# Optimization experiments

Hardware: AMD Instinct MI355X
Metric: run time of the kernel (lower is better)

The kernel has to match this reference:

```python
import jax, jax.numpy as jnp
import numpy as np
import math

D_MODEL = 768
B, S = 8, 2048


def setup_inputs() -> dict:
    key = jax.random.key(0)
    k1, k2, k3, k4, k5 = jax.random.split(key, 5)
    return {
        "input": jax.random.normal(k1, (B, S, D_MODEL), dtype=jnp.float32),
        "attention_mask": jax.random.randint(k2, (B,), 0, S + 1, dtype=jnp.int32),
        "Wq": jax.random.normal(k3, (D_MODEL, D_MODEL), dtype=jnp.float32),
        "Wk": jax.random.normal(k4, (D_MODEL, D_MODEL), dtype=jnp.float32),
        "Wv": jax.random.normal(k5, (D_MODEL, D_MODEL), dtype=jnp.float32),
    }


def reference(input, attention_mask, Wq, Wk, Wv):
    d_model = Wq.shape[0]
    # QKV projections (v is computed in the original but never used in the output)
    q = jnp.matmul(input, Wq)  # [B,S,D]
    k = jnp.matmul(input, Wk)  # [B,S,D]
    v = jnp.matmul(input, Wv)  # [B,S,D] (dead in original forward output)
    # Per-sample QK^T, vectorized instead of the original python loop+cat
    attention_score = jnp.einsum("bqd,bkd->bqk", q, k) / math.sqrt(float(d_model) ** 3)
    # Ragged mask: positions (j,k) with j<len_i and k<len_i keep the score, else -1000.
    # Built with vectorized arange comparisons instead of the original triple python loop.
    idx = jnp.arange(attention_score.shape[1])  # [S]
    valid = idx[None, :] < attention_mask[:, None]  # [B,S]
    keep = valid[:, :, None] & valid[:, None, :]  # [B,S,S]
    mask_attention_score = jnp.where(keep, attention_score, jnp.float32(-1000.0))
    attention_score_n = jax.nn.softmax(mask_attention_score, axis=-1)  # computed but unused, as in original
    # Original returns UNMASKED, pre-softmax scores matmul'd with the raw input (not v).
    self_attention = jnp.einsum("bqk,bkd->bqd", attention_score, input)
    return self_attention
```

## Files before the change

kernel.cpp:

```cpp
#include <hip/hip_runtime.h>
#include <hip/hip_bf16.h>
#include <cmath>


typedef __attribute__((ext_vector_type(8))) short short8;
typedef __attribute__((ext_vector_type(4))) float f32x4;

__device__ __forceinline__ unsigned short f2bf(float f) {
    union { float f; unsigned int u; } v; v.f = f;
    unsigned int u = v.u;
    return (unsigned short)((u + 0x7FFFu + ((u >> 16) & 1u)) >> 16);
}

__global__ __launch_bounds__(256)
void transpose_bf16(const float* __restrict__ X, unsigned short* __restrict__ Xt,
                    unsigned short* __restrict__ Xbf, int S, int D)
{
    __shared__ unsigned short tile[32][36];
    const int b = blockIdx.z;
    const int s0 = blockIdx.x * 32;
    const int d0 = blockIdx.y * 32;
    const float* Xb = X + (size_t)b * S * D;
    unsigned short* Xtb = Xt + (size_t)b * S * D;
    unsigned short* Xbb = Xbf + (size_t)b * S * D;
    const int tx = threadIdx.x & 7;
    const int ty = threadIdx.x >> 3;

    float4 v = *reinterpret_cast<const float4*>(&Xb[(size_t)(s0 + ty) * D + d0 + tx * 4]);
    ushort4 pk;
    pk.x = f2bf(v.x); pk.y = f2bf(v.y); pk.z = f2bf(v.z); pk.w = f2bf(v.w);
    *reinterpret_cast<ushort4*>(&Xbb[(size_t)(s0 + ty) * D + d0 + tx * 4]) = pk;
    tile[tx * 4 + 0][ty] = pk.x;
    tile[tx * 4 + 1][ty] = pk.y;
    tile[tx * 4 + 2][ty] = pk.z;
    tile[tx * 4 + 3][ty] = pk.w;
    __syncthreads();
    ushort4 o;
    o.x = tile[ty][tx * 4 + 0];
    o.y = tile[ty][tx * 4 + 1];
    o.z = tile[ty][tx * 4 + 2];
    o.w = tile[ty][tx * 4 + 3];
    *reinterpret_cast<ushort4*>(&Xtb[(size_t)(d0 + ty) * S + s0 + tx * 4]) = o;
}

template <int ROWS>
__device__ __forceinline__ void stage_glds(const unsigned short* src, unsigned short* lds,
                                           int ld, int tid)
{
    #pragma unroll
    for (int it = 0; it < ROWS / 32; ++it) {
        int slot = it * 256 + tid;
        int r = slot >> 3, c = slot & 7;
        const unsigned short* gp = src + (size_t)r * ld + ((c ^ (r & 7)) << 3);
        unsigned short* lp = lds + (size_t)(it * 256 + (tid & 192)) * 8;
        __builtin_amdgcn_global_load_lds(
            (__attribute__((address_space(1))) void*)(void*)gp,
            (__attribute__((address_space(3))) void*)lp, 16, 0, 0);
    }
}

template <int ROWS>
__device__ __forceinline__ void stage_f32(const float* src, unsigned short* lds,
                                          int ld, int tid)
{
    #pragma unroll
    for (int it = 0; it < ROWS / 32; ++it) {
        int slot = it * 256 + tid;
        int r = slot >> 3, c = slot & 7;
        const float* p = src + (size_t)r * ld + ((c ^ (r & 7)) << 3);
        float4 a = *reinterpret_cast<const float4*>(p);
        float4 b = *reinterpret_cast<const float4*>(p + 4);
        uint4 v;
        v.x = (unsigned)f2bf(a.x) | ((unsigned)f2bf(a.y) << 16);
        v.y = (unsigned)f2bf(a.z) | ((unsigned)f2bf(a.w) << 16);
        v.z = (unsigned)f2bf(b.x) | ((unsigned)f2bf(b.y) << 16);
        v.w = (unsigned)f2bf(b.z) | ((unsigned)f2bf(b.w) << 16);
        *reinterpret_cast<uint4*>(&lds[(size_t)slot * 8]) = v;
    }
}

__device__ __forceinline__ void store_c(float* C, size_t i, float v) { C[i] = v; }
__device__ __forceinline__ void store_c(unsigned short* C, size_t i, float v) { C[i] = f2bf(v); }

template <int TM, int TN, bool AF32, bool BF32, typename CT>
__global__ __launch_bounds__(256)
void gemm(const void* __restrict__ Ap, const void* __restrict__ Bp, CT* __restrict__ Cb,
          int Kloop, int lda, int ldb, int ldc, long sA, long sB, long sC, float alpha)
{
    constexpr int FM = TM / 32;
    constexpr int FN = TN / 32;
    const int b = blockIdx.z;
    CT* C = Cb + (long)b * sC;

    __shared__ unsigned short Alds[TM * 64];
    __shared__ unsigned short Blds[TN * 64];

    const int tid  = threadIdx.x;
    const int lane = tid & 63;
    const int wave = tid >> 6;
    const int wr   = (wave >> 1) * (TM / 2);
    const int wc   = (wave & 1) * (TN / 2);
    const int rowBase = blockIdx.x * TM;
    const int colBase = blockIdx.y * TN;
    const int l15  = lane & 15;
    const int quad = lane >> 4;

    f32x4 acc[FM][FN] = {};

    for (int k0 = 0; k0 < Kloop; k0 += 64) {
        if constexpr (AF32)
            stage_f32<TM>((const float*)Ap + (long)b * sA + (size_t)rowBase * lda + k0,
                          Alds, lda, tid);
        else
            stage_glds<TM>((const unsigned short*)Ap + (long)b * sA + (size_t)rowBase * lda + k0,
                           Alds, lda, tid);
        if constexpr (BF32)
            stage_f32<TN>((const float*)Bp + (long)b * sB + (size_t)colBase * ldb + k0,
                          Blds, ldb, tid);
        else
            stage_glds<TN>((const unsigned short*)Bp + (long)b * sB + (size_t)colBase * ldb + k0,
                           Blds, ldb, tid);
        __syncthreads();

        short8 af[FM][2], bfr[FN][2];
        #pragma unroll
        for (int i = 0; i < FM; ++i) {
            int ra = wr + i * 16 + l15;
            af[i][0] = *reinterpret_cast<const short8*>(&Alds[ra * 64 + ((quad ^ (ra & 7)) << 3)]);
            af[i][1] = *reinterpret_cast<const short8*>(&Alds[ra * 64 + (((quad + 4) ^ (ra & 7)) << 3)]);
        }
        #pragma unroll
        for (int i = 0; i < FN; ++i) {
            int rb = wc + i * 16 + l15;
            bfr[i][0] = *reinterpret_cast<const short8*>(&Blds[rb * 64 + ((quad ^ (rb & 7)) << 3)]);
            bfr[i][1] = *reinterpret_cast<const short8*>(&Blds[rb * 64 + (((quad + 4) ^ (rb & 7)) << 3)]);
        }
        #pragma unroll
        for (int ks = 0; ks < 2; ++ks)
            #pragma unroll
            for (int mi = 0; mi < FM; ++mi)
                #pragma unroll
                for (int ni = 0; ni < FN; ++ni)
                    acc[mi][ni] = __builtin_amdgcn_mfma_f32_16x16x32_bf16(
                        af[mi][ks], bfr[ni][ks], acc[mi][ni], 0, 0, 0);
        __syncthreads();
    }

    #pragma unroll
    for (int mi = 0; mi < FM; ++mi) {
        #pragma unroll
        for (int ni = 0; ni < FN; ++ni) {
            int col = colBase + wc + ni * 16 + l15;
            #pragma unroll
            for (int r = 0; r < 4; ++r) {
                int row = rowBase + wr + mi * 16 + quad * 4 + r;
                store_c(C, (size_t)row * ldc + col, alpha * acc[mi][ni][r]);
            }
        }
    }
}

extern "C" void kernel_launch(void* const* d_in, const int* in_sizes, int n_in,
                              void* d_out, int out_size, void* d_ws, size_t ws_size,
                              hipStream_t stream)
{
    const float* X  = (const float*)d_in[0];
    const float* Wq = (const float*)d_in[2];
    const float* Wk = (const float*)d_in[3];
    float* out = (float*)d_out;

    const int Bn = 8, S = 2048, D = 768;
    const float alpha = 1.0f / (768.0f * sqrtf(768.0f));
    const size_t szX  = (size_t)Bn * S * D;
    const size_t szDD = (size_t)Bn * D * D;

    unsigned short* Xt16 = (unsigned short*)d_ws;
    unsigned short* Xbf  = Xt16 + szX;
    unsigned short* P16  = Xbf + szX;
    unsigned short* G16  = P16 + (size_t)D * D;
    unsigned short* Ht16 = G16 + szDD;

    transpose_bf16<<<dim3(S / 32, D / 32, Bn), 256, 0, stream>>>(X, Xt16, Xbf, S, D);

    gemm<64, 64, true, true, unsigned short><<<dim3(12, 12, 1), 256, 0, stream>>>(
        Wq, Wk, P16, D, D, D, D, 0L, 0L, 0L, 1.0f);

    gemm<96, 96, false, false, unsigned short><<<dim3(8, 8, Bn), 256, 0, stream>>>(
        Xt16, Xt16, G16, S, S, S, D, (long)D * S, (long)D * S, (long)D * D, 1.0f);

    gemm<96, 96, false, false, unsigned short><<<dim3(8, 8, Bn), 256, 0, stream>>>(
        G16, P16, Ht16, D, D, D, D, (long)D * D, 0L, (long)D * D, alpha);

    gemm<128, 128, false, false, float><<<dim3(S / 128, 6, Bn), 256, 0, stream>>>(
        Xbf, Ht16, out, D, D, D, D, (long)S * D, (long)D * D, (long)S * D, 1.0f);
}
```

Baseline: 214.8 us.

## Pre-convert weights to bf16 and put batch on grid x for L2 reuse

Adds a separate kernel that converts Wq and Wk to bf16, so the weight-product GEMM can use async global-to-LDS loads instead of loading fp32 and converting inside the GEMM. It also moves the batch index to blockIdx.x so consecutively scheduled workgroups belong to different batches and share the same tile coordinates. The intent is to change how shared operands such as P16 and Ht16 are reused in L2, and to simplify the GEMM template. The cost is one extra launch and more workspace, and the new grid order could hurt locality for the per-batch operands.

```diff
diff --git a/kernel.cpp b/kernel.cpp
--- a/kernel.cpp
+++ b/kernel.cpp
@@ -10,6 +10,28 @@
     union { float f; unsigned int u; } v; v.f = f;
     unsigned int u = v.u;
     return (unsigned short)((u + 0x7FFFu + ((u >> 16) & 1u)) >> 16);
+}
+
+__global__ __launch_bounds__(256)
+void convert_w(const float* __restrict__ Wq, const float* __restrict__ Wk,
+               unsigned short* __restrict__ Wq16, unsigned short* __restrict__ Wk16)
+{
+    int i = (blockIdx.x * 256 + threadIdx.x) * 8;
+    float4 a = *reinterpret_cast<const float4*>(&Wq[i]);
+    float4 b = *reinterpret_cast<const float4*>(&Wq[i + 4]);
+    uint4 v;
+    v.x = (unsigned)f2bf(a.x) | ((unsigned)f2bf(a.y) << 16);
+    v.y = (unsigned)f2bf(a.z) | ((unsigned)f2bf(a.w) << 16);
+    v.z = (unsigned)f2bf(b.x) | ((unsigned)f2bf(b.y) << 16);
+    v.w = (unsigned)f2bf(b.z) | ((unsigned)f2bf(b.w) << 16);
+    *reinterpret_cast<uint4*>(&Wq16[i]) = v;
+    a = *reinterpret_cast<const float4*>(&Wk[i]);
+    b = *reinterpret_cast<const float4*>(&Wk[i + 4]);
+    v.x = (unsigned)f2bf(a.x) | ((unsigned)f2bf(a.y) << 16);
+    v.y = (unsigned)f2bf(a.z) | ((unsigned)f2bf(a.w) << 16);
+    v.z = (unsigned)f2bf(b.x) | ((unsigned)f2bf(b.y) << 16);
+    v.w = (unsigned)f2bf(b.z) | ((unsigned)f2bf(b.w) << 16);
+    *reinterpret_cast<uint4*>(&Wk16[i]) = v;
 }
 
 __global__ __launch_bounds__(256)
@@ -59,37 +81,18 @@
     }
 }
 
-template <int ROWS>
-__device__ __forceinline__ void stage_f32(const float* src, unsigned short* lds,
-                                          int ld, int tid)
-{
-    #pragma unroll
-    for (int it = 0; it < ROWS / 32; ++it) {
-        int slot = it * 256 + tid;
-        int r = slot >> 3, c = slot & 7;
-        const float* p = src + (size_t)r * ld + ((c ^ (r & 7)) << 3);
-        float4 a = *reinterpret_cast<const float4*>(p);
-        float4 b = *reinterpret_cast<const float4*>(p + 4);
-        uint4 v;
-        v.x = (unsigned)f2bf(a.x) | ((unsigned)f2bf(a.y) << 16);
-        v.y = (unsigned)f2bf(a.z) | ((unsigned)f2bf(a.w) << 16);
-        v.z = (unsigned)f2bf(b.x) | ((unsigned)f2bf(b.y) << 16);
-        v.w = (unsigned)f2bf(b.z) | ((unsigned)f2bf(b.w) << 16);
-        *reinterpret_cast<uint4*>(&lds[(size_t)slot * 8]) = v;
-    }
-}
-
 __device__ __forceinline__ void store_c(float* C, size_t i, float v) { C[i] = v; }
 __device__ __forceinline__ void store_c(unsigned short* C, size_t i, float v) { C[i] = f2bf(v); }
 
-template <int TM, int TN, bool AF32, bool BF32, typename CT>
+template <int TM, int TN, typename CT>
 __global__ __launch_bounds__(256)
-void gemm(const void* __restrict__ Ap, const void* __restrict__ Bp, CT* __restrict__ Cb,
+void gemm(const unsigned short* __restrict__ Ap, const unsigned short* __restrict__ Bp,
+          CT* __restrict__ Cb,
           int Kloop, int lda, int ldb, int ldc, long sA, long sB, long sC, float alpha)
 {
     constexpr int FM = TM / 32;
     constexpr int FN = TN / 32;
-    const int b = blockIdx.z;
+    const int b = blockIdx.x;
     CT* C = Cb + (long)b * sC;
 
     __shared__ unsigned short Alds[TM * 64];
@@ -100,26 +103,16 @@
     const int wave = tid >> 6;
     const int wr   = (wave >> 1) * (TM / 2);
     const int wc   = (wave & 1) * (TN / 2);
-    const int rowBase = blockIdx.x * TM;
-    const int colBase = blockIdx.y * TN;
+    const int rowBase = blockIdx.y * TM;
+    const int colBase = blockIdx.z * TN;
     const int l15  = lane & 15;
     const int quad = lane >> 4;
 
     f32x4 acc[FM][FN] = {};
 
     for (int k0 = 0; k0 < Kloop; k0 += 64) {
-        if constexpr (AF32)
-            stage_f32<TM>((const float*)Ap + (long)b * sA + (size_t)rowBase * lda + k0,
-                          Alds, lda, tid);
-        else
-            stage_glds<TM>((const unsigned short*)Ap + (long)b * sA + (size_t)rowBase * lda + k0,
-                           Alds, lda, tid);
-        if constexpr (BF32)
-            stage_f32<TN>((const float*)Bp + (long)b * sB + (size_t)colBase * ldb + k0,
-                          Blds, ldb, tid);
-        else
-            stage_glds<TN>((const unsigned short*)Bp + (long)b * sB + (size_t)colBase * ldb + k0,
-                           Blds, ldb, tid);
+        stage_glds<TM>(Ap + (long)b * sA + (size_t)rowBase * lda + k0, Alds, lda, tid);
+        stage_glds<TN>(Bp + (long)b * sB + (size_t)colBase * ldb + k0, Blds, ldb, tid);
         __syncthreads();
 
         short8 af[FM][2], bfr[FN][2];
@@ -179,18 +172,22 @@
     unsigned short* P16  = Xbf + szX;
     unsigned short* G16  = P16 + (size_t)D * D;
     unsigned short* Ht16 = G16 + szDD;
+    unsigned short* Wq16 = Ht16 + szDD;
+    unsigned short* Wk16 = Wq16 + (size_t)D * D;
+
+    convert_w<<<dim3(D * D / 2048, 1, 1), 256, 0, stream>>>(Wq, Wk, Wq16, Wk16);
 
     transpose_bf16<<<dim3(S / 32, D / 32, Bn), 256, 0, stream>>>(X, Xt16, Xbf, S, D);
 
-    gemm<64, 64, true, true, unsigned short><<<dim3(12, 12, 1), 256, 0, stream>>>(
-        Wq, Wk, P16, D, D, D, D, 0L, 0L, 0L, 1.0f);
+    gemm<64, 64, unsigned short><<<dim3(1, 12, 12), 256, 0, stream>>>(
+        Wq16, Wk16, P16, D, D, D, D, 0L, 0L, 0L, 1.0f);
 
-    gemm<96, 96, false, false, unsigned short><<<dim3(8, 8, Bn), 256, 0, stream>>>(
+    gemm<96, 96, unsigned short><<<dim3(Bn, 8, 8), 256, 0, stream>>>(
         Xt16, Xt16, G16, S, S, S, D, (long)D * S, (long)D * S, (long)D * D, 1.0f);
 
-    gemm<96, 96, false, false, unsigned short><<<dim3(8, 8, Bn), 256, 0, stream>>>(
+    gemm<96, 96, unsigned short><<<dim3(Bn, 8, 8), 256, 0, stream>>>(
         G16, P16, Ht16, D, D, D, D, (long)D * D, 0L, (long)D * D, alpha);
 
-    gemm<128, 128, false, false, float><<<dim3(S / 128, 6, Bn), 256, 0, stream>>>(
+    gemm<128, 128, float><<<dim3(Bn, S / 128, 6), 256, 0, stream>>>(
         Xbf, Ht16, out, D, D, D, D, (long)S * D, (long)D * D, (long)S * D, 1.0f);
 }
```

Result: faster. 189.9 us (-11.6%).
